# Kernel tuning notes

Hardware: AMD Instinct MI355X
Metric: run time of the kernel (lower is better)

## Reference

```python
import jax, jax.numpy as jnp
import numpy as np

HIDDEN = 1024
HEADS = 16
HEAD_DIM = HIDDEN // HEADS


def setup_inputs() -> dict:
    key = jax.random.key(0)
    ks = jax.random.split(key, 9)
    B, S = 4, 2048
    s = 1.0 / np.sqrt(HIDDEN)
    return {
        "inputs": jax.random.normal(ks[0], (B, S, HIDDEN), dtype=jnp.float32),
        "Wq": jax.random.normal(ks[1], (HIDDEN, HIDDEN), dtype=jnp.float32) * s,
        "bq": jnp.zeros((HIDDEN,), dtype=jnp.float32),
        "Wk": jax.random.normal(ks[2], (HIDDEN, HIDDEN), dtype=jnp.float32) * s,
        "bk": jnp.zeros((HIDDEN,), dtype=jnp.float32),
        "Wv": jax.random.normal(ks[3], (HIDDEN, HIDDEN), dtype=jnp.float32) * s,
        "bv": jnp.zeros((HIDDEN,), dtype=jnp.float32),
        "Wp": jax.random.normal(ks[4], (HIDDEN, HIDDEN), dtype=jnp.float32) * s,
        "bp": jnp.zeros((HIDDEN,), dtype=jnp.float32),
        "heads_z": jnp.ones((1, HEADS, 1, 1), dtype=jnp.float32),
        "hidden_z": jnp.ones((HIDDEN,), dtype=jnp.float32),
    }


def _split_heads(x):
    # [B,S,HIDDEN] -> [B,H,S,Dh]
    B, S, _ = x.shape
    return x.reshape(B, S, HEADS, HEAD_DIM).transpose(0, 2, 1, 3)


def reference(inputs, Wq, bq, Wk, bk, Wv, bv, Wp, bp, heads_z, hidden_z):
    q = _split_heads(inputs @ Wq.T + bq)
    k = _split_heads(inputs @ Wk.T + bk)
    v = _split_heads(inputs @ Wv.T + bv)
    scores = jnp.einsum("bhqd,bhkd->bhqk", q, k) / jnp.sqrt(
        jnp.asarray(HEAD_DIM, dtype=q.dtype))
    probs = jax.nn.softmax(scores, axis=-1)
    ctx = jnp.einsum("bhqk,bhkd->bhqd", probs, v)  # [B,H,S,Dh]
    ctx = ctx * heads_z
    B, H, S, D = ctx.shape
    ctx = ctx.transpose(0, 2, 1, 3).reshape(B, S, H * D)
    out = ctx @ Wp.T + bp
    out = out * hidden_z
    return out
```

## Files before the change

### kernel.cpp

```cpp
#include <hip/hip_runtime.h>
#include <hip/hip_bf16.h>

#define HID 1024
#define NH 16
#define DH 64
#define SEQ 2048
#define NB 4
#define MTOT (NB*SEQ)

typedef __attribute__((ext_vector_type(4))) float f32x4;
typedef __attribute__((ext_vector_type(16))) float f32x16;
typedef __attribute__((ext_vector_type(8))) __bf16 bf16x8;
typedef __attribute__((ext_vector_type(4))) __bf16 bf16x4;
typedef __attribute__((ext_vector_type(2))) __bf16 bf16x2;
typedef __attribute__((ext_vector_type(2))) int i32x2;

__device__ __forceinline__ f32x4 mfma16(bf16x8 a, bf16x8 b, f32x4 c) {
    return __builtin_amdgcn_mfma_f32_16x16x32_bf16(a, b, c, 0, 0, 0);
}
__device__ __forceinline__ f32x16 mfma32(bf16x8 a, bf16x8 b, f32x16 c) {
    return __builtin_amdgcn_mfma_f32_32x32x16_bf16(a, b, c, 0, 0, 0);
}

__device__ __forceinline__ void gload16(const void* g, void* l) {
    __builtin_amdgcn_global_load_lds(
        (const __attribute__((address_space(1))) unsigned int*)g,
        (__attribute__((address_space(3))) unsigned int*)l, 16, 0, 0);
}

__device__ __forceinline__ float fexp2(float x) {
#if __has_builtin(__builtin_amdgcn_exp2f)
    return __builtin_amdgcn_exp2f(x);
#else
    return exp2f(x);
#endif
}

__device__ __forceinline__ unsigned pkbf2(float lo, float hi) {
    union { bf16x2 v; unsigned u; } c;
    c.v = (bf16x2){ (__bf16)lo, (__bf16)hi };
    return c.u;
}

__device__ __forceinline__ void swap32(unsigned &a, unsigned &b) {
#if __has_builtin(__builtin_amdgcn_permlane32_swap)
    i32x2 r = __builtin_amdgcn_permlane32_swap((int)a, (int)b, false, false);
    a = (unsigned)r.x; b = (unsigned)r.y;
#else
    const bool hi = (threadIdx.x & 32) != 0;
    unsigned ta = __shfl_xor(a, 32), tb = __shfl_xor(b, 32);
    unsigned na = hi ? tb : a;
    unsigned nb = hi ? b : ta;
    a = na; b = nb;
#endif
}

__device__ __forceinline__ float swapmaxf(float x) {
    unsigned a = __float_as_uint(x), b = a;
    swap32(a, b);
    return fmaxf(__uint_as_float(a), __uint_as_float(b));
}
__device__ __forceinline__ float swapaddf(float x) {
    unsigned a = __float_as_uint(x), b = a;
    swap32(a, b);
    return __uint_as_float(a) + __uint_as_float(b);
}

__global__ __launch_bounds__(256)
void cvt(const float* __restrict__ in, __bf16* __restrict__ out, int n) {
    int i = (blockIdx.x * 256 + threadIdx.x) * 4;
    if (i >= n) return;
    float4 v = *(const float4*)(in + i);
    bf16x4 o = { (__bf16)v.x, (__bf16)v.y, (__bf16)v.z, (__bf16)v.w };
    *(bf16x4*)(out + i) = o;
}

template<int MODE>
__global__ __launch_bounds__(256)
void gemm_bt(const __bf16* __restrict__ A, const __bf16* __restrict__ W,
             const float* __restrict__ bias, const float* __restrict__ hz,
             void* __restrict__ outp)
{
    __shared__ __bf16 As[128 * 32];
    __shared__ __bf16 Bs[128 * 32];
    const int tid  = threadIdx.x;
    const int lane = tid & 63, wid = tid >> 6;
    const int m0 = blockIdx.x * 128;
    const int n0 = blockIdx.y * 128;
    const int wm = (wid >> 1) * 64, wn = (wid & 1) * 64;

    f32x4 acc[4][4];
    #pragma unroll
    for (int i = 0; i < 4; i++)
        #pragma unroll
        for (int j = 0; j < 4; j++) acc[i][j] = (f32x4){0.f, 0.f, 0.f, 0.f};

    for (int kt = 0; kt < HID; kt += 32) {
        #pragma unroll
        for (int i = 0; i < 2; i++) {
            int c = wid * 128 + i * 64 + lane;
            int row = c >> 2, slot = c & 3;
            int ss = slot ^ (row & 3);
            gload16(A + (size_t)(m0 + row) * HID + kt + ss * 8, (char*)As + c * 16);
            gload16(W + (size_t)(n0 + row) * HID + kt + ss * 8, (char*)Bs + c * 16);
        }
        __syncthreads();

        bf16x8 af[4], bfr[4];
        #pragma unroll
        for (int mi = 0; mi < 4; mi++) {
            int row = wm + mi * 16 + (lane & 15);
            int off = row * 64 + (((lane >> 4) * 16) ^ ((row & 3) << 4));
            af[mi] = *(const bf16x8*)((const char*)As + off);
        }
        #pragma unroll
        for (int ni = 0; ni < 4; ni++) {
            int row = wn + ni * 16 + (lane & 15);
            int off = row * 64 + (((lane >> 4) * 16) ^ ((row & 3) << 4));
            bfr[ni] = *(const bf16x8*)((const char*)Bs + off);
        }
        #pragma unroll
        for (int mi = 0; mi < 4; mi++)
            #pragma unroll
            for (int ni = 0; ni < 4; ni++)
                acc[mi][ni] = mfma16(af[mi], bfr[ni], acc[mi][ni]);
        __syncthreads();
    }

    #pragma unroll
    for (int mi = 0; mi < 4; mi++)
        #pragma unroll
        for (int ni = 0; ni < 4; ni++)
            #pragma unroll
            for (int r = 0; r < 4; r++) {
                int m = m0 + wm + mi * 16 + ((lane >> 4) * 4) + r;
                int n = n0 + wn + ni * 16 + (lane & 15);
                float v = acc[mi][ni][r] + bias[n];
                if (MODE == 3) {
                    ((float*)outp)[(size_t)m * HID + n] = v * hz[n];
                } else {
                    int b = m >> 11, s = m & (SEQ - 1);
                    int h = n >> 6,  d = n & 63;
                    size_t idx;
                    if (MODE == 2) idx = ((size_t)(b * NH + h) * DH + d) * SEQ + s;
                    else           idx = ((size_t)(b * NH + h) * SEQ + s) * DH + d;
                    ((__bf16*)outp)[idx] = (__bf16)v;
                }
            }
}

#define KVB 64
#define SM_SCALE 0.18033688f

__global__ __launch_bounds__(512, 4)
void attn(const __bf16* __restrict__ Q, const __bf16* __restrict__ K,
          const __bf16* __restrict__ VT, const float* __restrict__ heads_z,
          __bf16* __restrict__ C)
{
    __shared__ __bf16 Ks[2][KVB * 64];
    __shared__ __bf16 Vs[2][KVB * 64];
    const int tid = threadIdx.x, lane = tid & 63, wid = tid >> 6;
    const int lh = lane >> 5;
    const int qb = blockIdx.x, hd = blockIdx.y, b = blockIdx.z;
    const size_t bh = (size_t)(b * NH + hd);
    const __bf16* Qg = Q + bh * SEQ * DH;
    const __bf16* Kg = K + bh * SEQ * DH;
    const __bf16* Vg = VT + bh * (size_t)DH * SEQ;
    const int q0 = qb * 256;
    const int q = q0 + wid * 32 + (lane & 31);

    bf16x8 qf[4];
    #pragma unroll
    for (int s = 0; s < 4; s++)
        qf[s] = *(const bf16x8*)(Qg + (size_t)q * DH + s * 16 + lh * 8);

    f32x16 ctx0, ctx1;
    #pragma unroll
    for (int r = 0; r < 16; r++) { ctx0[r] = 0.f; ctx1[r] = 0.f; }
    float mrun = -1e30f, lrun = 0.f;

    const int sc_row = tid >> 3, sc_slot = tid & 7;
    const int sc_ss = sc_slot ^ (sc_row & 7);

    gload16(Kg + (size_t)sc_row * DH + sc_ss * 8, (char*)&Ks[0][0] + tid * 16);
    gload16(Vg + (size_t)sc_row * SEQ + 0 + sc_ss * 8, (char*)&Vs[0][0] + tid * 16);
    __syncthreads();

    int cur = 0;
    for (int kv0 = 0; kv0 < SEQ; kv0 += KVB) {
        if (kv0 + KVB < SEQ) {
            gload16(Kg + (size_t)(kv0 + KVB + sc_row) * DH + sc_ss * 8,
                    (char*)&Ks[cur ^ 1][0] + tid * 16);
            gload16(Vg + (size_t)sc_row * SEQ + (kv0 + KVB) + sc_ss * 8,
                    (char*)&Vs[cur ^ 1][0] + tid * 16);
        }

        f32x16 st0, st1;
        #pragma unroll
        for (int r = 0; r < 16; r++) { st0[r] = 0.f; st1[r] = 0.f; }
        const char* Kb = (const char*)&Ks[cur][0];
        __builtin_amdgcn_s_setprio(1);
        #pragma unroll
        for (int s = 0; s < 4; s++) {
            int r0 = lane & 31, r1 = r0 + 32;
            int slot = 2 * s + lh;
            bf16x8 k0 = *(const bf16x8*)(Kb + r0 * 128 + ((slot ^ (r0 & 7)) << 4));
            bf16x8 k1 = *(const bf16x8*)(Kb + r1 * 128 + ((slot ^ (r1 & 7)) << 4));
            st0 = mfma32(k0, qf[s], st0);
            st1 = mfma32(k1, qf[s], st1);
        }
        __builtin_amdgcn_s_setprio(0);

        float pm = st0[0];
        #pragma unroll
        for (int r = 1; r < 16; r++) pm = fmaxf(pm, st0[r]);
        #pragma unroll
        for (int r = 0; r < 16; r++) pm = fmaxf(pm, st1[r]);
        pm = swapmaxf(pm);
        pm *= SM_SCALE;
        if (!__all(pm <= mrun + 8.f)) {
            float nm = fmaxf(mrun, pm);
            float al = fexp2(mrun - nm);
            lrun *= al; mrun = nm;
            #pragma unroll
            for (int r = 0; r < 16; r++) { ctx0[r] *= al; ctx1[r] *= al; }
        }
        float rs = 0.f;
        const float mneg = -mrun;
        #pragma unroll
        for (int r = 0; r < 16; r++) {
            float e0 = fexp2(fmaf(st0[r], SM_SCALE, mneg));
            float e1 = fexp2(fmaf(st1[r], SM_SCALE, mneg));
            st0[r] = e0; st1[r] = e1;
            rs += e0 + e1;
        }
        lrun += swapaddf(rs);

        unsigned X0 = pkbf2(st0[0],  st0[1]),  X1 = pkbf2(st0[2],  st0[3]);
        unsigned X2 = pkbf2(st0[4],  st0[5]),  X3 = pkbf2(st0[6],  st0[7]);
        unsigned X4 = pkbf2(st0[8],  st0[9]),  X5 = pkbf2(st0[10], st0[11]);
        unsigned X6 = pkbf2(st0[12], st0[13]), X7 = pkbf2(st0[14], st0[15]);
        unsigned Y0 = pkbf2(st1[0],  st1[1]),  Y1 = pkbf2(st1[2],  st1[3]);
        unsigned Y2 = pkbf2(st1[4],  st1[5]),  Y3 = pkbf2(st1[6],  st1[7]);
        unsigned Y4 = pkbf2(st1[8],  st1[9]),  Y5 = pkbf2(st1[10], st1[11]);
        unsigned Y6 = pkbf2(st1[12], st1[13]), Y7 = pkbf2(st1[14], st1[15]);
        swap32(X0, X2); swap32(X1, X3);
        swap32(X4, X6); swap32(X5, X7);
        swap32(Y0, Y2); swap32(Y1, Y3);
        swap32(Y4, Y6); swap32(Y5, Y7);
        union W4 { unsigned w[4]; bf16x8 v; };
        W4 pf[4];
        pf[0].w[0]=X0; pf[0].w[1]=X1; pf[0].w[2]=X2; pf[0].w[3]=X3;
        pf[1].w[0]=X4; pf[1].w[1]=X5; pf[1].w[2]=X6; pf[1].w[3]=X7;
        pf[2].w[0]=Y0; pf[2].w[1]=Y1; pf[2].w[2]=Y2; pf[2].w[3]=Y3;
        pf[3].w[0]=Y4; pf[3].w[1]=Y5; pf[3].w[2]=Y6; pf[3].w[3]=Y7;

        const char* Vb = (const char*)&Vs[cur][0];
        __builtin_amdgcn_s_setprio(1);
        #pragma unroll
        for (int s = 0; s < 4; s++) {
            int r0 = lane & 31, r1 = r0 + 32;
            int slot = 2 * s + lh;
            bf16x8 v0 = *(const bf16x8*)(Vb + r0 * 128 + ((slot ^ (r0 & 7)) << 4));
            bf16x8 v1 = *(const bf16x8*)(Vb + r1 * 128 + ((slot ^ (r1 & 7)) << 4));
            ctx0 = mfma32(v0, pf[s].v, ctx0);
            ctx1 = mfma32(v1, pf[s].v, ctx1);
        }
        __builtin_amdgcn_s_setprio(0);

        __syncthreads();
        cur ^= 1;
    }

    const float hzv = heads_z[hd];
    const float rl = hzv / lrun;
    __bf16* Crow = C + (size_t)(b * SEQ + q) * HID + hd * DH;
    #pragma unroll
    for (int g = 0; g < 4; g++) {
        bf16x4 o0, o1;
        #pragma unroll
        for (int j = 0; j < 4; j++) {
            o0[j] = (__bf16)(ctx0[4 * g + j] * rl);
            o1[j] = (__bf16)(ctx1[4 * g + j] * rl);
        }
        int d0 = 8 * g + 4 * lh;
        *(bf16x4*)(Crow + d0) = o0;
        *(bf16x4*)(Crow + 32 + d0) = o1;
    }
}

extern "C" void kernel_launch(void* const* d_in, const int* in_sizes, int n_in,
                              void* d_out, int out_size, void* d_ws, size_t ws_size,
                              hipStream_t stream)
{
    const float* X    = (const float*)d_in[0];
    const float* Wq   = (const float*)d_in[1];
    const float* bq   = (const float*)d_in[2];
    const float* Wk   = (const float*)d_in[3];
    const float* bk   = (const float*)d_in[4];
    const float* Wv   = (const float*)d_in[5];
    const float* bv   = (const float*)d_in[6];
    const float* Wp   = (const float*)d_in[7];
    const float* bp   = (const float*)d_in[8];
    const float* hz   = (const float*)d_in[9];
    const float* hidz = (const float*)d_in[10];

    __bf16* ws  = (__bf16*)d_ws;
    __bf16* Xb  = ws;
    __bf16* Wqb = Xb  + (size_t)MTOT * HID;
    __bf16* Wkb = Wqb + (size_t)HID * HID;
    __bf16* Wvb = Wkb + (size_t)HID * HID;
    __bf16* Wpb = Wvb + (size_t)HID * HID;
    __bf16* Qb  = Wpb + (size_t)HID * HID;
    __bf16* Kb  = Qb  + (size_t)MTOT * HID;
    __bf16* VTb = Kb  + (size_t)MTOT * HID;
    __bf16* Cb  = VTb + (size_t)MTOT * HID;

    cvt<<<(MTOT * HID / 4 + 255) / 256, 256, 0, stream>>>(X,  Xb,  MTOT * HID);
    cvt<<<(HID * HID / 4 + 255) / 256, 256, 0, stream>>>(Wq, Wqb, HID * HID);
    cvt<<<(HID * HID / 4 + 255) / 256, 256, 0, stream>>>(Wk, Wkb, HID * HID);
    cvt<<<(HID * HID / 4 + 255) / 256, 256, 0, stream>>>(Wv, Wvb, HID * HID);
    cvt<<<(HID * HID / 4 + 255) / 256, 256, 0, stream>>>(Wp, Wpb, HID * HID);

    dim3 gg(MTOT / 128, HID / 128);
    gemm_bt<0><<<gg, 256, 0, stream>>>(Xb, Wqb, bq, nullptr, Qb);
    gemm_bt<1><<<gg, 256, 0, stream>>>(Xb, Wkb, bk, nullptr, Kb);
    gemm_bt<2><<<gg, 256, 0, stream>>>(Xb, Wvb, bv, nullptr, VTb);

    attn<<<dim3(SEQ / 256, NH, NB), 512, 0, stream>>>(Qb, Kb, VTb, hz, Cb);

    gemm_bt<3><<<gg, 256, 0, stream>>>(Cb, Wpb, bp, hidz, d_out);
}
```

Before: 220.3 us.

## Merge conversion and QKV launches, enlarge attention KV tile, remap attention grid

The five fp32-to-bf16 conversion launches become one grid-strided kernel, and the three QKV projection GEMMs become one launch that picks Q/K/V from blockIdx.z. The goal is less launch overhead and better fill of the device. The attention kernel now stages 128 keys per shared-memory buffer, processed as two 64-key halves, which halves the number of barriers. It also uses a 1D grid with a remapped block index so that blocks of the same head tend to run together and share K/V in cache. The max and sum reductions are restructured into trees to shorten dependency chains. The cost is double the LDS use per attention block, which may limit the intended 4 blocks per CU.

```diff
diff --git a/kernel.cpp b/kernel.cpp
--- a/kernel.cpp
+++ b/kernel.cpp
@@ -67,19 +67,110 @@
 }
 
 __global__ __launch_bounds__(256)
-void cvt(const float* __restrict__ in, __bf16* __restrict__ out, int n) {
-    int i = (blockIdx.x * 256 + threadIdx.x) * 4;
-    if (i >= n) return;
-    float4 v = *(const float4*)(in + i);
-    bf16x4 o = { (__bf16)v.x, (__bf16)v.y, (__bf16)v.z, (__bf16)v.w };
-    *(bf16x4*)(out + i) = o;
-}
-
-template<int MODE>
+void cvt5(const float* __restrict__ X,  const float* __restrict__ Wq,
+          const float* __restrict__ Wk, const float* __restrict__ Wv,
+          const float* __restrict__ Wp,
+          __bf16* __restrict__ Xb,  __bf16* __restrict__ Wqb,
+          __bf16* __restrict__ Wkb, __bf16* __restrict__ Wvb,
+          __bf16* __restrict__ Wpb)
+{
+    const float* src; __bf16* dst; int n;
+    switch (blockIdx.y) {
+        case 0:  src = X;  dst = Xb;  n = MTOT * HID; break;
+        case 1:  src = Wq; dst = Wqb; n = HID * HID;  break;
+        case 2:  src = Wk; dst = Wkb; n = HID * HID;  break;
+        case 3:  src = Wv; dst = Wvb; n = HID * HID;  break;
+        default: src = Wp; dst = Wpb; n = HID * HID;  break;
+    }
+    const int stride = gridDim.x * 256 * 4;
+    for (int i = (blockIdx.x * 256 + threadIdx.x) * 4; i < n; i += stride) {
+        float4 v = *(const float4*)(src + i);
+        bf16x4 o = { (__bf16)v.x, (__bf16)v.y, (__bf16)v.z, (__bf16)v.w };
+        *(bf16x4*)(dst + i) = o;
+    }
+}
+
 __global__ __launch_bounds__(256)
-void gemm_bt(const __bf16* __restrict__ A, const __bf16* __restrict__ W,
-             const float* __restrict__ bias, const float* __restrict__ hz,
-             void* __restrict__ outp)
+void gemm_qkv(const __bf16* __restrict__ A,
+              const __bf16* __restrict__ Wq, const __bf16* __restrict__ Wk,
+              const __bf16* __restrict__ Wv,
+              const float* __restrict__ bq, const float* __restrict__ bk,
+              const float* __restrict__ bv,
+              __bf16* __restrict__ Qo, __bf16* __restrict__ Ko, __bf16* __restrict__ Vo)
+{
+    __shared__ __bf16 As[128 * 32];
+    __shared__ __bf16 Bs[128 * 32];
+    const int mode = blockIdx.z;
+    const __bf16* W    = mode == 0 ? Wq : mode == 1 ? Wk : Wv;
+    const float*  bias = mode == 0 ? bq : mode == 1 ? bk : bv;
+    __bf16*       Og   = mode == 0 ? Qo : mode == 1 ? Ko : Vo;
+
+    const int tid  = threadIdx.x;
+    const int lane = tid & 63, wid = tid >> 6;
+    const int m0 = blockIdx.x * 128;
+    const int n0 = blockIdx.y * 128;
+    const int wm = (wid >> 1) * 64, wn = (wid & 1) * 64;
+
+    f32x4 acc[4][4];
+    #pragma unroll
+    for (int i = 0; i < 4; i++)
+        #pragma unroll
+        for (int j = 0; j < 4; j++) acc[i][j] = (f32x4){0.f, 0.f, 0.f, 0.f};
+
+    for (int kt = 0; kt < HID; kt += 32) {
+        #pragma unroll
+        for (int i = 0; i < 2; i++) {
+            int c = wid * 128 + i * 64 + lane;
+            int row = c >> 2, slot = c & 3;
+            int ss = slot ^ (row & 3);
+            gload16(A + (size_t)(m0 + row) * HID + kt + ss * 8, (char*)As + c * 16);
+            gload16(W + (size_t)(n0 + row) * HID + kt + ss * 8, (char*)Bs + c * 16);
+        }
+        __syncthreads();
+
+        bf16x8 af[4], bfr[4];
+        #pragma unroll
+        for (int mi = 0; mi < 4; mi++) {
+            int row = wm + mi * 16 + (lane & 15);
+            int off = row * 64 + (((lane >> 4) * 16) ^ ((row & 3) << 4));
+            af[mi] = *(const bf16x8*)((const char*)As + off);
+        }
+        #pragma unroll
+        for (int ni = 0; ni < 4; ni++) {
+            int row = wn + ni * 16 + (lane & 15);
+            int off = row * 64 + (((lane >> 4) * 16) ^ ((row & 3) << 4));
+            bfr[ni] = *(const bf16x8*)((const char*)Bs + off);
+        }
+        #pragma unroll
+        for (int mi = 0; mi < 4; mi++)
+            #pragma unroll
+            for (int ni = 0; ni < 4; ni++)
+                acc[mi][ni] = mfma16(af[mi], bfr[ni], acc[mi][ni]);
+        __syncthreads();
+    }
+
+    #pragma unroll
+    for (int mi = 0; mi < 4; mi++)
+        #pragma unroll
+        for (int ni = 0; ni < 4; ni++)
+            #pragma unroll
+            for (int r = 0; r < 4; r++) {
+                int m = m0 + wm + mi * 16 + ((lane >> 4) * 4) + r;
+                int n = n0 + wn + ni * 16 + (lane & 15);
+                float v = acc[mi][ni][r] + bias[n];
+                int b = m >> 11, s = m & (SEQ - 1);
+                int h = n >> 6,  d = n & 63;
+                size_t idx;
+                if (mode == 2) idx = ((size_t)(b * NH + h) * DH + d) * SEQ + s;
+                else           idx = ((size_t)(b * NH + h) * SEQ + s) * DH + d;
+                Og[idx] = (__bf16)v;
+            }
+}
+
+__global__ __launch_bounds__(256)
+void gemm_proj(const __bf16* __restrict__ A, const __bf16* __restrict__ W,
+               const float* __restrict__ bias, const float* __restrict__ hz,
+               float* __restrict__ outp)
 {
     __shared__ __bf16 As[128 * 32];
     __shared__ __bf16 Bs[128 * 32];
@@ -135,21 +226,11 @@
             for (int r = 0; r < 4; r++) {
                 int m = m0 + wm + mi * 16 + ((lane >> 4) * 4) + r;
                 int n = n0 + wn + ni * 16 + (lane & 15);
-                float v = acc[mi][ni][r] + bias[n];
-                if (MODE == 3) {
-                    ((float*)outp)[(size_t)m * HID + n] = v * hz[n];
-                } else {
-                    int b = m >> 11, s = m & (SEQ - 1);
-                    int h = n >> 6,  d = n & 63;
-                    size_t idx;
-                    if (MODE == 2) idx = ((size_t)(b * NH + h) * DH + d) * SEQ + s;
-                    else           idx = ((size_t)(b * NH + h) * SEQ + s) * DH + d;
-                    ((__bf16*)outp)[idx] = (__bf16)v;
-                }
-            }
-}
-
-#define KVB 64
+                outp[(size_t)m * HID + n] = (acc[mi][ni][r] + bias[n]) * hz[n];
+            }
+}
+
+#define KVB 128
 #define SM_SCALE 0.18033688f
 
 __global__ __launch_bounds__(512, 4)
@@ -158,16 +239,20 @@
           __bf16* __restrict__ C)
 {
     __shared__ __bf16 Ks[2][KVB * 64];
-    __shared__ __bf16 Vs[2][KVB * 64];
+    __shared__ __bf16 Vs[2][64 * KVB];
     const int tid = threadIdx.x, lane = tid & 63, wid = tid >> 6;
     const int lh = lane >> 5;
-    const int qb = blockIdx.x, hd = blockIdx.y, b = blockIdx.z;
-    const size_t bh = (size_t)(b * NH + hd);
-    const __bf16* Qg = Q + bh * SEQ * DH;
-    const __bf16* Kg = K + bh * SEQ * DH;
-    const __bf16* Vg = VT + bh * (size_t)DH * SEQ;
-    const int q0 = qb * 256;
-    const int q = q0 + wid * 32 + (lane & 31);
+    const int id = blockIdx.x;
+    const int bh = (id & 7) | ((id >> 6) << 3);
+    const int qb = (id >> 3) & 7;
+    const int b = bh >> 4, hd = bh & 15;
+    const __bf16* Qg = Q + (size_t)bh * SEQ * DH;
+    const __bf16* Kg = K + (size_t)bh * SEQ * DH;
+    const __bf16* Vg = VT + (size_t)bh * DH * SEQ;
+    const int q = qb * 256 + wid * 32 + (lane & 31);
+    const int r0 = lane & 31;
+    const int kx = (r0 & 7) << 4;
+    const int vx = (r0 & 15) << 4;
 
     bf16x8 qf[4];
     #pragma unroll
@@ -179,94 +264,108 @@
     for (int r = 0; r < 16; r++) { ctx0[r] = 0.f; ctx1[r] = 0.f; }
     float mrun = -1e30f, lrun = 0.f;
 
-    const int sc_row = tid >> 3, sc_slot = tid & 7;
-    const int sc_ss = sc_slot ^ (sc_row & 7);
-
-    gload16(Kg + (size_t)sc_row * DH + sc_ss * 8, (char*)&Ks[0][0] + tid * 16);
-    gload16(Vg + (size_t)sc_row * SEQ + 0 + sc_ss * 8, (char*)&Vs[0][0] + tid * 16);
+    const int kr0 = tid >> 3,          ksl0 = tid & 7,          kss0 = ksl0 ^ (kr0 & 7);
+    const int kr1 = (tid + 512) >> 3,  ksl1 = tid & 7,          kss1 = ksl1 ^ (kr1 & 7);
+    const int vr0 = tid >> 4,          vsl0 = tid & 15,         vss0 = vsl0 ^ (vr0 & 15);
+    const int vr1 = (tid + 512) >> 4,  vsl1 = tid & 15,         vss1 = vsl1 ^ (vr1 & 15);
+
+    {
+        gload16(Kg + (size_t)kr0 * DH + kss0 * 8, (char*)&Ks[0][0] + tid * 16);
+        gload16(Kg + (size_t)kr1 * DH + kss1 * 8, (char*)&Ks[0][0] + (tid + 512) * 16);
+        gload16(Vg + (size_t)vr0 * SEQ + 0 + vss0 * 8, (char*)&Vs[0][0] + tid * 16);
+        gload16(Vg + (size_t)vr1 * SEQ + 0 + vss1 * 8, (char*)&Vs[0][0] + (tid + 512) * 16);
+    }
     __syncthreads();
 
     int cur = 0;
     for (int kv0 = 0; kv0 < SEQ; kv0 += KVB) {
         if (kv0 + KVB < SEQ) {
-            gload16(Kg + (size_t)(kv0 + KVB + sc_row) * DH + sc_ss * 8,
-                    (char*)&Ks[cur ^ 1][0] + tid * 16);
-            gload16(Vg + (size_t)sc_row * SEQ + (kv0 + KVB) + sc_ss * 8,
-                    (char*)&Vs[cur ^ 1][0] + tid * 16);
-        }
-
-        f32x16 st0, st1;
-        #pragma unroll
-        for (int r = 0; r < 16; r++) { st0[r] = 0.f; st1[r] = 0.f; }
-        const char* Kb = (const char*)&Ks[cur][0];
-        __builtin_amdgcn_s_setprio(1);
-        #pragma unroll
-        for (int s = 0; s < 4; s++) {
-            int r0 = lane & 31, r1 = r0 + 32;
-            int slot = 2 * s + lh;
-            bf16x8 k0 = *(const bf16x8*)(Kb + r0 * 128 + ((slot ^ (r0 & 7)) << 4));
-            bf16x8 k1 = *(const bf16x8*)(Kb + r1 * 128 + ((slot ^ (r1 & 7)) << 4));
-            st0 = mfma32(k0, qf[s], st0);
-            st1 = mfma32(k1, qf[s], st1);
-        }
-        __builtin_amdgcn_s_setprio(0);
-
-        float pm = st0[0];
-        #pragma unroll
-        for (int r = 1; r < 16; r++) pm = fmaxf(pm, st0[r]);
-        #pragma unroll
-        for (int r = 0; r < 16; r++) pm = fmaxf(pm, st1[r]);
-        pm = swapmaxf(pm);
-        pm *= SM_SCALE;
-        if (!__all(pm <= mrun + 8.f)) {
-            float nm = fmaxf(mrun, pm);
-            float al = fexp2(mrun - nm);
-            lrun *= al; mrun = nm;
-            #pragma unroll
-            for (int r = 0; r < 16; r++) { ctx0[r] *= al; ctx1[r] *= al; }
-        }
-        float rs = 0.f;
-        const float mneg = -mrun;
-        #pragma unroll
-        for (int r = 0; r < 16; r++) {
-            float e0 = fexp2(fmaf(st0[r], SM_SCALE, mneg));
-            float e1 = fexp2(fmaf(st1[r], SM_SCALE, mneg));
-            st0[r] = e0; st1[r] = e1;
-            rs += e0 + e1;
-        }
-        lrun += swapaddf(rs);
-
-        unsigned X0 = pkbf2(st0[0],  st0[1]),  X1 = pkbf2(st0[2],  st0[3]);
-        unsigned X2 = pkbf2(st0[4],  st0[5]),  X3 = pkbf2(st0[6],  st0[7]);
-        unsigned X4 = pkbf2(st0[8],  st0[9]),  X5 = pkbf2(st0[10], st0[11]);
-        unsigned X6 = pkbf2(st0[12], st0[13]), X7 = pkbf2(st0[14], st0[15]);
-        unsigned Y0 = pkbf2(st1[0],  st1[1]),  Y1 = pkbf2(st1[2],  st1[3]);
-        unsigned Y2 = pkbf2(st1[4],  st1[5]),  Y3 = pkbf2(st1[6],  st1[7]);
-        unsigned Y4 = pkbf2(st1[8],  st1[9]),  Y5 = pkbf2(st1[10], st1[11]);
-        unsigned Y6 = pkbf2(st1[12], st1[13]), Y7 = pkbf2(st1[14], st1[15]);
-        swap32(X0, X2); swap32(X1, X3);
-        swap32(X4, X6); swap32(X5, X7);
-        swap32(Y0, Y2); swap32(Y1, Y3);
-        swap32(Y4, Y6); swap32(Y5, Y7);
-        union W4 { unsigned w[4]; bf16x8 v; };
-        W4 pf[4];
-        pf[0].w[0]=X0; pf[0].w[1]=X1; pf[0].w[2]=X2; pf[0].w[3]=X3;
-        pf[1].w[0]=X4; pf[1].w[1]=X5; pf[1].w[2]=X6; pf[1].w[3]=X7;
-        pf[2].w[0]=Y0; pf[2].w[1]=Y1; pf[2].w[2]=Y2; pf[2].w[3]=Y3;
-        pf[3].w[0]=Y4; pf[3].w[1]=Y5; pf[3].w[2]=Y6; pf[3].w[3]=Y7;
-
-        const char* Vb = (const char*)&Vs[cur][0];
-        __builtin_amdgcn_s_setprio(1);
-        #pragma unroll
-        for (int s = 0; s < 4; s++) {
-            int r0 = lane & 31, r1 = r0 + 32;
-            int slot = 2 * s + lh;
-            bf16x8 v0 = *(const bf16x8*)(Vb + r0 * 128 + ((slot ^ (r0 & 7)) << 4));
-            bf16x8 v1 = *(const bf16x8*)(Vb + r1 * 128 + ((slot ^ (r1 & 7)) << 4));
-            ctx0 = mfma32(v0, pf[s].v, ctx0);
-            ctx1 = mfma32(v1, pf[s].v, ctx1);
-        }
-        __builtin_amdgcn_s_setprio(0);
+            int nx = kv0 + KVB;
+            gload16(Kg + (size_t)(nx + kr0) * DH + kss0 * 8, (char*)&Ks[cur ^ 1][0] + tid * 16);
+            gload16(Kg + (size_t)(nx + kr1) * DH + kss1 * 8, (char*)&Ks[cur ^ 1][0] + (tid + 512) * 16);
+            gload16(Vg + (size_t)vr0 * SEQ + nx + vss0 * 8, (char*)&Vs[cur ^ 1][0] + tid * 16);
+            gload16(Vg + (size_t)vr1 * SEQ + nx + vss1 * 8, (char*)&Vs[cur ^ 1][0] + (tid + 512) * 16);
+        }
+
+        #pragma unroll
+        for (int hh = 0; hh < 2; hh++) {
+            const char* Kb = (const char*)&Ks[cur][0] + hh * 64 * 128;
+            const char* Vb = (const char*)&Vs[cur][0];
+
+            f32x16 st0, st1;
+            #pragma unroll
+            for (int r = 0; r < 16; r++) { st0[r] = 0.f; st1[r] = 0.f; }
+            __builtin_amdgcn_s_setprio(1);
+            #pragma unroll
+            for (int s = 0; s < 4; s++) {
+                int co = (2 * s + lh) << 4;
+                bf16x8 k0 = *(const bf16x8*)(Kb + r0 * 128 + (co ^ kx));
+                bf16x8 k1 = *(const bf16x8*)(Kb + (r0 + 32) * 128 + (co ^ kx));
+                st0 = mfma32(k0, qf[s], st0);
+                st1 = mfma32(k1, qf[s], st1);
+            }
+            __builtin_amdgcn_s_setprio(0);
+
+            float t8[8];
+            #pragma unroll
+            for (int j = 0; j < 8; j++)
+                t8[j] = fmaxf(fmaxf(st0[2 * j], st0[2 * j + 1]),
+                              fmaxf(st1[2 * j], st1[2 * j + 1]));
+            float t4a = fmaxf(t8[0], t8[1]), t4b = fmaxf(t8[2], t8[3]);
+            float t4c = fmaxf(t8[4], t8[5]), t4d = fmaxf(t8[6], t8[7]);
+            float pm = fmaxf(fmaxf(t4a, t4b), fmaxf(t4c, t4d));
+            pm = swapmaxf(pm);
+            pm *= SM_SCALE;
+            if (!__all(pm <= mrun + 8.f)) {
+                float nm = fmaxf(mrun, pm);
+                float al = fexp2(mrun - nm);
+                lrun *= al; mrun = nm;
+                #pragma unroll
+                for (int r = 0; r < 16; r++) { ctx0[r] *= al; ctx1[r] *= al; }
+            }
+            const float mneg = -mrun;
+            float rsA = 0.f, rsB = 0.f, rsC = 0.f, rsD = 0.f;
+            #pragma unroll
+            for (int r = 0; r < 16; r += 2) {
+                float e0 = fexp2(fmaf(st0[r],     SM_SCALE, mneg));
+                float e1 = fexp2(fmaf(st0[r + 1], SM_SCALE, mneg));
+                float e2 = fexp2(fmaf(st1[r],     SM_SCALE, mneg));
+                float e3 = fexp2(fmaf(st1[r + 1], SM_SCALE, mneg));
+                st0[r] = e0; st0[r + 1] = e1; st1[r] = e2; st1[r + 1] = e3;
+                rsA += e0; rsB += e1; rsC += e2; rsD += e3;
+            }
+            lrun += swapaddf((rsA + rsB) + (rsC + rsD));
+
+            unsigned X0 = pkbf2(st0[0],  st0[1]),  X1 = pkbf2(st0[2],  st0[3]);
+            unsigned X2 = pkbf2(st0[4],  st0[5]),  X3 = pkbf2(st0[6],  st0[7]);
+            unsigned X4 = pkbf2(st0[8],  st0[9]),  X5 = pkbf2(st0[10], st0[11]);
+            unsigned X6 = pkbf2(st0[12], st0[13]), X7 = pkbf2(st0[14], st0[15]);
+            unsigned Y0 = pkbf2(st1[0],  st1[1]),  Y1 = pkbf2(st1[2],  st1[3]);
+            unsigned Y2 = pkbf2(st1[4],  st1[5]),  Y3 = pkbf2(st1[6],  st1[7]);
+            unsigned Y4 = pkbf2(st1[8],  st1[9]),  Y5 = pkbf2(st1[10], st1[11]);
+            unsigned Y6 = pkbf2(st1[12], st1[13]), Y7 = pkbf2(st1[14], st1[15]);
+            swap32(X0, X2); swap32(X1, X3);
+            swap32(X4, X6); swap32(X5, X7);
+            swap32(Y0, Y2); swap32(Y1, Y3);
+            swap32(Y4, Y6); swap32(Y5, Y7);
+            union W4 { unsigned w[4]; bf16x8 v; };
+            W4 pf[4];
+            pf[0].w[0]=X0; pf[0].w[1]=X1; pf[0].w[2]=X2; pf[0].w[3]=X3;
+            pf[1].w[0]=X4; pf[1].w[1]=X5; pf[1].w[2]=X6; pf[1].w[3]=X7;
+            pf[2].w[0]=Y0; pf[2].w[1]=Y1; pf[2].w[2]=Y2; pf[2].w[3]=Y3;
+            pf[3].w[0]=Y4; pf[3].w[1]=Y5; pf[3].w[2]=Y6; pf[3].w[3]=Y7;
+
+            __builtin_amdgcn_s_setprio(1);
+            #pragma unroll
+            for (int s = 0; s < 4; s++) {
+                int co = (hh * 8 + 2 * s + lh) << 4;
+                bf16x8 v0 = *(const bf16x8*)(Vb + r0 * 256 + (co ^ vx));
+                bf16x8 v1 = *(const bf16x8*)(Vb + (r0 + 32) * 256 + (co ^ vx));
+                ctx0 = mfma32(v0, pf[s].v, ctx0);
+                ctx1 = mfma32(v1, pf[s].v, ctx1);
+            }
+            __builtin_amdgcn_s_setprio(0);
+        }
 
         __syncthreads();
         cur ^= 1;
@@ -316,18 +415,12 @@
     __bf16* VTb = Kb  + (size_t)MTOT * HID;
     __bf16* Cb  = VTb + (size_t)MTOT * HID;
 
-    cvt<<<(MTOT * HID / 4 + 255) / 256, 256, 0, stream>>>(X,  Xb,  MTOT * HID);
-    cvt<<<(HID * HID / 4 + 255) / 256, 256, 0, stream>>>(Wq, Wqb, HID * HID);
-    cvt<<<(HID * HID / 4 + 255) / 256, 256, 0, stream>>>(Wk, Wkb, HID * HID);
-    cvt<<<(HID * HID / 4 + 255) / 256, 256, 0, stream>>>(Wv, Wvb, HID * HID);
-    cvt<<<(HID * HID / 4 + 255) / 256, 256, 0, stream>>>(Wp, Wpb, HID * HID);
-
-    dim3 gg(MTOT / 128, HID / 128);
-    gemm_bt<0><<<gg, 256, 0, stream>>>(Xb, Wqb, bq, nullptr, Qb);
-    gemm_bt<1><<<gg, 256, 0, stream>>>(Xb, Wkb, bk, nullptr, Kb);
-    gemm_bt<2><<<gg, 256, 0, stream>>>(Xb, Wvb, bv, nullptr, VTb);
-
-    attn<<<dim3(SEQ / 256, NH, NB), 512, 0, stream>>>(Qb, Kb, VTb, hz, Cb);
-
-    gemm_bt<3><<<gg, 256, 0, stream>>>(Cb, Wpb, bp, hidz, d_out);
-}
+    cvt5<<<dim3(2048, 5), 256, 0, stream>>>(X, Wq, Wk, Wv, Wp, Xb, Wqb, Wkb, Wvb, Wpb);
+
+    gemm_qkv<<<dim3(MTOT / 128, HID / 128, 3), 256, 0, stream>>>(
+        Xb, Wqb, Wkb, Wvb, bq, bk, bv, Qb, Kb, VTb);
+
+    attn<<<dim3(512), 512, 0, stream>>>(Qb, Kb, VTb, hz, Cb);
+
+    gemm_proj<<<dim3(MTOT / 128, HID / 128), 256, 0, stream>>>(Cb, Wpb, bp, hidz, (float*)d_out);
+}
```

Result: faster. 209.7 us (-4.8%).
